# Kernel tuning notes

Hardware: AMD Instinct MI355X
Metric: run time of the kernel (lower is better)

The kernel has to match this reference:

```python
import jax, jax.numpy as jnp
import numpy as np

OUT_H = 7
OUT_W = 7
SPATIAL_SCALE = 0.25
SAMPLING_RATIO = 2  # exact sampling branch (sampling_ratio > 0)
ALIGNED = True


def setup_inputs() -> dict:
    key = jax.random.key(0)
    k1, k2, k3, k4 = jax.random.split(key, 4)
    feat = jax.random.normal(k1, (4, 256, 100, 100), dtype=jnp.float32)
    # rois[K,5]: (batch_idx, x1, y1, x2, y2) in image coords (image ~400px since scale=0.25)
    K = 512
    bidx = jax.random.randint(k2, (K,), 0, 4).astype(jnp.float32)
    xy1 = jax.random.uniform(k3, (K, 2), minval=0.0, maxval=300.0, dtype=jnp.float32)
    wh = jax.random.uniform(k4, (K, 2), minval=20.0, maxval=99.0, dtype=jnp.float32)
    xy2 = xy1 + wh
    rois = jnp.concatenate([bidx[:, None], xy1[:, 0:1], xy1[:, 1:2], xy2[:, 0:1], xy2[:, 1:2]], axis=1)
    return {"input": feat, "rois": rois}


def _roi_align(feat, rois):
    N, C, H, W = feat.shape
    b = rois[:, 0].astype(jnp.int32)  # [K]
    offset = 0.5 if ALIGNED else 0.0
    sw = rois[:, 1] * SPATIAL_SCALE - offset
    sh = rois[:, 2] * SPATIAL_SCALE - offset
    ew = rois[:, 3] * SPATIAL_SCALE - offset
    eh = rois[:, 4] * SPATIAL_SCALE - offset
    rw = ew - sw
    rh = eh - sh
    if not ALIGNED:
        rw = jnp.maximum(rw, 1.0)
        rh = jnp.maximum(rh, 1.0)
    bin_h = rh / OUT_H  # [K]
    bin_w = rw / OUT_W

    ph = jnp.arange(OUT_H, dtype=feat.dtype)
    pw = jnp.arange(OUT_W, dtype=feat.dtype)
    samp = jnp.arange(SAMPLING_RATIO, dtype=feat.dtype) + 0.5  # (i + 0.5)

    # y: [K, OUT_H, SR], x: [K, OUT_W, SR]
    y = sh[:, None, None] + ph[None, :, None] * bin_h[:, None, None] + samp[None, None, :] * (bin_h / SAMPLING_RATIO)[:, None, None]
    x = sw[:, None, None] + pw[None, :, None] * bin_w[:, None, None] + samp[None, None, :] * (bin_w / SAMPLING_RATIO)[:, None, None]

    # bilinear interpolation indices/weights (matches _bilinear_interpolate)
    y = jnp.maximum(y, 0.0)
    x = jnp.maximum(x, 0.0)
    yl = y.astype(jnp.int32)
    xl = x.astype(jnp.int32)
    yh = jnp.where(yl >= H - 1, H - 1, yl + 1)
    yl = jnp.where(yl >= H - 1, H - 1, yl)
    xh = jnp.where(xl >= W - 1, W - 1, xl + 1)
    xl = jnp.where(xl >= W - 1, W - 1, xl)
    ly = y - yl.astype(feat.dtype)
    lx = x - xl.astype(feat.dtype)
    hy = 1.0 - ly
    hx = 1.0 - lx

    def gather(yi, xi):
        # yi: [K,PH,IY], xi: [K,PW,IX] -> [K,PH,IY,PW,IX,C]
        return feat[b[:, None, None, None, None], :,
                    yi[:, :, :, None, None],
                    xi[:, None, None, :, :]]

    v1 = gather(yl, xl)
    v2 = gather(yl, xh)
    v3 = gather(yh, xl)
    v4 = gather(yh, xh)

    out = (jnp.einsum('kpi,kqj,kpiqjc->kcpq', hy, hx, v1)
           + jnp.einsum('kpi,kqj,kpiqjc->kcpq', hy, lx, v2)
           + jnp.einsum('kpi,kqj,kpiqjc->kcpq', ly, hx, v3)
           + jnp.einsum('kpi,kqj,kpiqjc->kcpq', ly, lx, v4))
    count = float(max(SAMPLING_RATIO * SAMPLING_RATIO, 1))
    return out / count  # [K, C, OUT_H, OUT_W]


def reference(input, rois):
    return _roi_align(input, rois)
```

## Files before the change

kernel.cpp:

```cpp
#include <hip/hip_runtime.h>


#define FEAT_C 256
#define FEAT_H 100
#define FEAT_W 100
#define HW     (FEAT_H * FEAT_W)
#define NROI   512
#define PHOUT  7
#define PWOUT  7
#define SR     2
#define NBINS  (PHOUT * PWOUT)
#define CPB    8
#define GROUPS (FEAT_C / CPB)
#define SCALE  0.25f
#define PMAX   26
#define PSTR   27
#define CSTR   (PSTR * PMAX)

__device__ __forceinline__ void samp_geo(float s, float binsz, int idx, int sr_i,
                                         int cap, int& lo, float& fr) {
    float v = s + binsz * ((float)idx + ((float)sr_i + 0.5f) * 0.5f);
    v = fmaxf(v, 0.0f);
    int l = (int)v;
    if (l > cap) l = cap;
    fr = v - (float)l;
    lo = l;
}

__global__ __launch_bounds__(256) void roialign_fwd(
    const float* __restrict__ feat,
    const float* __restrict__ rois,
    float* __restrict__ out)
{
    __shared__ float s_patch[CPB * CSTR];
    __shared__ int2  s_yg[PHOUT * SR];
    __shared__ int2  s_xg[PWOUT * SR];

    const int bid = blockIdx.x;
    const int k   = bid >> 5;
    const int cg  = bid & (GROUPS - 1);
    const int tid = threadIdx.x;

    const float* r = rois + k * 5;
    const int   b  = (int)r[0];
    const float sw = r[1] * SCALE - 0.5f;
    const float sh = r[2] * SCALE - 0.5f;
    const float ew = r[3] * SCALE - 0.5f;
    const float eh = r[4] * SCALE - 0.5f;
    const float bin_h = (eh - sh) * (1.0f / PHOUT);
    const float bin_w = (ew - sw) * (1.0f / PWOUT);

    int y0, x0, yM, xM; float frd;
    samp_geo(sh, bin_h, 0,         0,      FEAT_H - 1, y0, frd);
    samp_geo(sh, bin_h, PHOUT - 1, SR - 1, FEAT_H - 1, yM, frd);
    samp_geo(sw, bin_w, 0,         0,      FEAT_W - 1, x0, frd);
    samp_geo(sw, bin_w, PWOUT - 1, SR - 1, FEAT_W - 1, xM, frd);
    const int ph_rows = min(yM - y0 + 2, PMAX);
    const int pw_cols = min(xM - x0 + 2, PMAX);

    if (tid < PHOUT * SR) {
        int lo; float ly;
        samp_geo(sh, bin_h, tid >> 1, tid & 1, FEAT_H - 1, lo, ly);
        s_yg[tid] = make_int2((lo - y0) * PSTR, __float_as_int(ly));
    } else if (tid >= 32 && tid < 32 + PWOUT * SR) {
        int t = tid - 32;
        int lo; float lx;
        samp_geo(sw, bin_w, t >> 1, t & 1, FEAT_W - 1, lo, lx);
        s_xg[t] = make_int2(lo - x0, __float_as_int(lx));
    }

    const float* fbase = feat + ((size_t)b * FEAT_C + cg * CPB) * HW;
    const int tx   = tid & 31;
    const int trow = tid >> 5;
    if (tx < pw_cols) {
        int sx = x0 + tx; if (sx > FEAT_W - 1) sx = FEAT_W - 1;
        for (int py = trow; py < ph_rows; py += 8) {
            int sy = y0 + py; if (sy > FEAT_H - 1) sy = FEAT_H - 1;
            const float* fp = fbase + sy * FEAT_W + sx;
            float*       dp = s_patch + py * PSTR + tx;
            #pragma unroll
            for (int c = 0; c < CPB; c++)
                dp[c * CSTR] = fp[c * HW];
        }
    }
    __syncthreads();

    float* obase = out + ((size_t)k * FEAT_C + cg * CPB) * NBINS;
    for (int o = tid; o < CPB * NBINS; o += 256) {
        int c   = o / NBINS;
        int bin = o - c * NBINS;
        int ph  = bin / PWOUT;
        int pw  = bin - ph * PWOUT;
        const float* p = s_patch + c * CSTR;

        int2  xg0 = s_xg[pw * 2 + 0];
        int2  xg1 = s_xg[pw * 2 + 1];
        float lx0 = __int_as_float(xg0.y), hx0 = 1.0f - lx0;
        float lx1 = __int_as_float(xg1.y), hx1 = 1.0f - lx1;

        float acc = 0.0f;
        #pragma unroll
        for (int iy = 0; iy < SR; iy++) {
            int2  yg = s_yg[ph * 2 + iy];
            float ly = __int_as_float(yg.y), hy = 1.0f - ly;
            const float* row = p + yg.x;

            const float* q0 = row + xg0.x;
            float v1 = q0[0], v2 = q0[1];
            float v3 = q0[PSTR], v4 = q0[PSTR + 1];
            acc += hy * (hx0 * v1 + lx0 * v2) + ly * (hx0 * v3 + lx0 * v4);

            const float* q1 = row + xg1.x;
            v1 = q1[0]; v2 = q1[1];
            v3 = q1[PSTR]; v4 = q1[PSTR + 1];
            acc += hy * (hx1 * v1 + lx1 * v2) + ly * (hx1 * v3 + lx1 * v4);
        }
        obase[o] = acc * 0.25f;
    }
}

extern "C" void kernel_launch(void* const* d_in, const int* in_sizes, int n_in,
                              void* d_out, int out_size, void* d_ws, size_t ws_size,
                              hipStream_t stream) {
    const float* feat = (const float*)d_in[0];
    const float* rois = (const float*)d_in[1];
    float*       outp = (float*)d_out;
    roialign_fwd<<<dim3(NROI * GROUPS), dim3(256), 0, stream>>>(feat, rois, outp);
}
```

Baseline: 108.9 us.

## Vectorize patch loads with float4 and compute two channels per thread

```diff
diff --git a/kernel.cpp b/kernel.cpp
--- a/kernel.cpp
+++ b/kernel.cpp
@@ -8,14 +8,15 @@
 #define NROI   512
 #define PHOUT  7
 #define PWOUT  7
-#define SR     2
-#define NBINS  (PHOUT * PWOUT)
+#define NBINS  49
 #define CPB    8
 #define GROUPS (FEAT_C / CPB)
 #define SCALE  0.25f
-#define PMAX   26
-#define PSTR   27
-#define CSTR   (PSTR * PMAX)
+#define PROWS  25
+#define PSTR   28
+#define CSTR   (PSTR * PROWS)
+
+typedef float f32x2 __attribute__((ext_vector_type(2)));
 
 __device__ __forceinline__ void samp_geo(float s, float binsz, int idx, int sr_i,
                                          int cap, int& lo, float& fr) {
@@ -32,9 +33,10 @@
     const float* __restrict__ rois,
     float* __restrict__ out)
 {
-    __shared__ float s_patch[CPB * CSTR];
-    __shared__ int2  s_yg[PHOUT * SR];
-    __shared__ int2  s_xg[PWOUT * SR];
+    __shared__ __align__(16) float s_patch[CPB * CSTR];
+    __shared__ __align__(16) int2  s_yg[PHOUT * 2];
+    __shared__ __align__(16) int2  s_xg[PWOUT * 2];
+    __shared__ int2 s_bm[NBINS];
 
     const int bid = blockIdx.x;
     const int k   = bid >> 5;
@@ -47,75 +49,95 @@
     const float sh = r[2] * SCALE - 0.5f;
     const float ew = r[3] * SCALE - 0.5f;
     const float eh = r[4] * SCALE - 0.5f;
-    const float bin_h = (eh - sh) * (1.0f / PHOUT);
-    const float bin_w = (ew - sw) * (1.0f / PWOUT);
+    const float bh = (eh - sh) * (1.0f / PHOUT);
+    const float bw = (ew - sw) * (1.0f / PWOUT);
 
-    int y0, x0, yM, xM; float frd;
-    samp_geo(sh, bin_h, 0,         0,      FEAT_H - 1, y0, frd);
-    samp_geo(sh, bin_h, PHOUT - 1, SR - 1, FEAT_H - 1, yM, frd);
-    samp_geo(sw, bin_w, 0,         0,      FEAT_W - 1, x0, frd);
-    samp_geo(sw, bin_w, PWOUT - 1, SR - 1, FEAT_W - 1, xM, frd);
-    const int ph_rows = min(yM - y0 + 2, PMAX);
-    const int pw_cols = min(xM - x0 + 2, PMAX);
+    int y0, x0, yM, xM; float fd;
+    samp_geo(sh, bh, 0,         0, FEAT_H - 1, y0, fd);
+    samp_geo(sh, bh, PHOUT - 1, 1, FEAT_H - 1, yM, fd);
+    samp_geo(sw, bw, 0,         0, FEAT_W - 1, x0, fd);
+    samp_geo(sw, bw, PWOUT - 1, 1, FEAT_W - 1, xM, fd);
+    const int  ax0     = x0 & ~3;
+    const int  ph_rows = min(yM - y0 + 2, PROWS);
+    const int  aspan   = min(xM - ax0 + 2, PSTR);
+    const bool dupx    = (xM >= FEAT_W - 1);
 
-    if (tid < PHOUT * SR) {
-        int lo; float ly;
-        samp_geo(sh, bin_h, tid >> 1, tid & 1, FEAT_H - 1, lo, ly);
-        s_yg[tid] = make_int2((lo - y0) * PSTR, __float_as_int(ly));
-    } else if (tid >= 32 && tid < 32 + PWOUT * SR) {
-        int t = tid - 32;
-        int lo; float lx;
-        samp_geo(sw, bin_w, t >> 1, t & 1, FEAT_W - 1, lo, lx);
-        s_xg[t] = make_int2(lo - x0, __float_as_int(lx));
+    if (tid < PHOUT * 2) {
+        int lo; float fr;
+        samp_geo(sh, bh, tid >> 1, tid & 1, FEAT_H - 1, lo, fr);
+        s_yg[tid] = make_int2((lo - y0) * PSTR, __float_as_int(fr));
+    } else if (tid >= 32 && tid < 32 + PWOUT * 2) {
+        int t = tid - 32; int lo; float fr;
+        samp_geo(sw, bw, t >> 1, t & 1, FEAT_W - 1, lo, fr);
+        s_xg[t] = make_int2(lo - ax0, __float_as_int(fr));
+    } else if (tid >= 64 && tid < 64 + NBINS) {
+        int bin = tid - 64;
+        s_bm[bin] = make_int2((bin / PWOUT) * 2, (bin % PWOUT) * 2);
     }
 
-    const float* fbase = feat + ((size_t)b * FEAT_C + cg * CPB) * HW;
-    const int tx   = tid & 31;
-    const int trow = tid >> 5;
-    if (tx < pw_cols) {
-        int sx = x0 + tx; if (sx > FEAT_W - 1) sx = FEAT_W - 1;
-        for (int py = trow; py < ph_rows; py += 8) {
-            int sy = y0 + py; if (sy > FEAT_H - 1) sy = FEAT_H - 1;
-            const float* fp = fbase + sy * FEAT_W + sx;
-            float*       dp = s_patch + py * PSTR + tx;
+    const float* fb = feat + ((size_t)b * FEAT_C + cg * CPB) * HW;
+    {
+        const int py = tid >> 3;
+        const int q  = tid & 7;
+        if (py < ph_rows && q * 4 < aspan) {
+            int qs = ax0 + q * 4;
+            if (qs > FEAT_W - 4) qs = FEAT_W - 4;
+            int sy = y0 + py;
+            if (sy > FEAT_H - 1) sy = FEAT_H - 1;
+            const float* src = fb + sy * FEAT_W + qs;
+            float*       dst = s_patch + py * PSTR + (qs - ax0);
             #pragma unroll
             for (int c = 0; c < CPB; c++)
-                dp[c * CSTR] = fp[c * HW];
+                *reinterpret_cast<float4*>(dst + c * CSTR) =
+                    *reinterpret_cast<const float4*>(src + c * HW);
         }
     }
     __syncthreads();
 
-    float* obase = out + ((size_t)k * FEAT_C + cg * CPB) * NBINS;
-    for (int o = tid; o < CPB * NBINS; o += 256) {
-        int c   = o / NBINS;
-        int bin = o - c * NBINS;
-        int ph  = bin / PWOUT;
-        int pw  = bin - ph * PWOUT;
-        const float* p = s_patch + c * CSTR;
+    if (dupx) {
+        int c = tid >> 5, py = tid & 31;
+        if (py < ph_rows) {
+            float* pr = s_patch + c * CSTR + py * PSTR;
+            pr[aspan - 1] = pr[aspan - 2];
+        }
+    }
+    __syncthreads();
 
-        int2  xg0 = s_xg[pw * 2 + 0];
-        int2  xg1 = s_xg[pw * 2 + 1];
-        float lx0 = __int_as_float(xg0.y), hx0 = 1.0f - lx0;
-        float lx1 = __int_as_float(xg1.y), hx1 = 1.0f - lx1;
+    if (tid < 4 * NBINS) {
+        const int cp  = tid / NBINS;
+        const int bin = tid - cp * NBINS;
+        const int2 bm = s_bm[bin];
+        const int4 yg = *reinterpret_cast<const int4*>(&s_yg[bm.x]);
+        const int4 xg = *reinterpret_cast<const int4*>(&s_xg[bm.y]);
+        const float* pA = s_patch + (cp * 2) * CSTR;
+        const float* pB = pA + CSTR;
 
-        float acc = 0.0f;
-        #pragma unroll
-        for (int iy = 0; iy < SR; iy++) {
-            int2  yg = s_yg[ph * 2 + iy];
-            float ly = __int_as_float(yg.y), hy = 1.0f - ly;
-            const float* row = p + yg.x;
+        const float ly0 = __int_as_float(yg.y), hy0 = 1.0f - ly0;
+        const float ly1 = __int_as_float(yg.w), hy1 = 1.0f - ly1;
+        const float lx0 = __int_as_float(xg.y), hx0 = 1.0f - lx0;
+        const float lx1 = __int_as_float(xg.w), hx1 = 1.0f - lx1;
 
-            const float* q0 = row + xg0.x;
-            float v1 = q0[0], v2 = q0[1];
-            float v3 = q0[PSTR], v4 = q0[PSTR + 1];
-            acc += hy * (hx0 * v1 + lx0 * v2) + ly * (hx0 * v3 + lx0 * v4);
+        f32x2 acc = {0.0f, 0.0f};
+        auto quad = [&](int ro, float hy, float ly, int xo, float hx, float lx) {
+            const float* a = pA + ro + xo;
+            const float* q = pB + ro + xo;
+            f32x2 vL0 = {a[0],        q[0]};
+            f32x2 vL1 = {a[1],        q[1]};
+            f32x2 vH0 = {a[PSTR],     q[PSTR]};
+            f32x2 vH1 = {a[PSTR + 1], q[PSTR + 1]};
+            f32x2 t = vL0 * hx + vL1 * lx;
+            f32x2 u = vH0 * hx + vH1 * lx;
+            acc += t * hy + u * ly;
+        };
+        quad(yg.x, hy0, ly0, xg.x, hx0, lx0);
+        quad(yg.x, hy0, ly0, xg.z, hx1, lx1);
+        quad(yg.z, hy1, ly1, xg.x, hx0, lx0);
+        quad(yg.z, hy1, ly1, xg.z, hx1, lx1);
+        acc *= 0.25f;
 
-            const float* q1 = row + xg1.x;
-            v1 = q1[0]; v2 = q1[1];
-            v3 = q1[PSTR]; v4 = q1[PSTR + 1];
-            acc += hy * (hx1 * v1 + lx1 * v2) + ly * (hx1 * v3 + lx1 * v4);
-        }
-        obase[o] = acc * 0.25f;
+        float* ob = out + ((size_t)k * FEAT_C + cg * CPB + cp * 2) * NBINS + bin;
+        ob[0]     = acc.x;
+        ob[NBINS] = acc.y;
     }
 }
 
```

Result: faster. 105.4 us (-3.2%).
